# Optimization experiments

Hardware: AMD Instinct MI355X
Metric: run time of the kernel (lower is better)

The kernel has to match this reference:

```python
import jax, jax.numpy as jnp
import numpy as np

B, N, E, H = 2, 2048, 1024, 16
HD = E // H  # head_dim = 64


def setup_inputs() -> dict:
    key = jax.random.key(0)
    k1, k2, k3, k4, k5 = jax.random.split(key, 5)
    x = jax.random.normal(k1, (B, N, E), dtype=jnp.float32)
    # per-head Linear(E, 3*HD): stacked weights [H, E, 3*HD] and biases [H, 3*HD]
    Wqkv = jax.random.normal(k2, (H, E, 3 * HD), dtype=jnp.float32) * (1.0 / np.sqrt(E))
    bqkv = jax.random.normal(k3, (H, 3 * HD), dtype=jnp.float32) * 0.01
    Wout = jax.random.normal(k4, (E, E), dtype=jnp.float32) * (1.0 / np.sqrt(E))
    bout = jax.random.normal(k5, (E,), dtype=jnp.float32) * 0.01
    return {"x": x, "Wqkv": Wqkv, "bqkv": bqkv, "Wout": Wout, "bout": bout}


def reference(x, Wqkv, bqkv, Wout, bout):
    # per-head QKV projection, vectorized over heads: [B, H, N, 3*HD]
    proj = jnp.einsum('bne,hef->bhnf', x, Wqkv) + bqkv[None, :, None, :]
    k, q, v = jnp.split(proj, 3, axis=-1)  # each [B, H, N, HD]
    # scores = q @ k^T / sqrt(HD): [B, H, N, N]
    scores = jnp.einsum('bhqd,bhkd->bhqk', q, k) / jnp.sqrt(jnp.asarray(HD, dtype=x.dtype))
    # causal mask (tril)
    causal = jnp.tril(jnp.ones((N, N), dtype=bool))
    scores = jnp.where(causal[None, None, :, :], scores, -jnp.inf)
    attn = jax.nn.softmax(scores, axis=-1)
    sa = jnp.einsum('bhqk,bhkd->bhqd', attn, v)  # [B, H, N, HD]
    # concat heads in order -> [B, N, E]
    sa = jnp.transpose(sa, (0, 2, 1, 3)).reshape(B, N, E)
    return sa @ Wout + bout
```

## Files before the change

### kernel.cpp

```cpp
#include <hip/hip_runtime.h>
#include <hip/hip_bf16.h>

#define Bz 2
#define Nn 2048
#define Ee 1024
#define Hh 16
#define HD 64

typedef unsigned short u16;
typedef unsigned int u32;

typedef __bf16 bf16x8 __attribute__((ext_vector_type(8)));
typedef float f32x4 __attribute__((ext_vector_type(4)));

#define QK_SCALE 0.18033688f

__device__ __forceinline__ float bf2f(u16 u) {
    u32 v = ((u32)u) << 16;
    return __builtin_bit_cast(float, v);
}
__device__ __forceinline__ u16 f2bf(float f) {
    u32 i = __builtin_bit_cast(u32, f);
    u32 r = (i + 0x7FFFu + ((i >> 16) & 1u)) >> 16;
    return (u16)r;
}
__device__ __forceinline__ u32 pack2(float a, float b) {
    return (u32)f2bf(a) | ((u32)f2bf(b) << 16);
}
__device__ __forceinline__ u32 pack2h(float a, float b) {
    u32 ua = __builtin_bit_cast(u32, a) + 0x8000u;
    u32 ub = __builtin_bit_cast(u32, b) + 0x8000u;
    return (ua >> 16) | (ub & 0xFFFF0000u);
}
__device__ __forceinline__ bf16x8 ld_frag(const u16* p) {
    return __builtin_bit_cast(bf16x8, *(const uint4*)p);
}
__device__ __forceinline__ f32x4 zero4() {
    f32x4 z; z[0]=0.f; z[1]=0.f; z[2]=0.f; z[3]=0.f; return z;
}

__device__ __forceinline__ void async_copy16(const u16* g, u16* l) {
    __builtin_amdgcn_global_load_lds(
        (const __attribute__((address_space(1))) u32*)g,
        (__attribute__((address_space(3))) u32*)l, 16, 0, 0);
}

__global__ void ws_diag(float* out, float code) { out[0] = code; }

__global__ __launch_bounds__(256) void convert_x(
    const float* __restrict__ x, u16* __restrict__ xbf)
{
    size_t idx = ((size_t)blockIdx.x * 256 + threadIdx.x) * 8;
    float4 f0 = *(const float4*)(x + idx);
    float4 f1 = *(const float4*)(x + idx + 4);
    uint4 pk;
    pk.x = pack2(f0.x, f0.y); pk.y = pack2(f0.z, f0.w);
    pk.z = pack2(f1.x, f1.y); pk.w = pack2(f1.z, f1.w);
    *(uint4*)(xbf + idx) = pk;
}

__global__ __launch_bounds__(256) void transpose_f32_bf16(
    const float* __restrict__ src, u16* __restrict__ dst, int R, int C)
{
    const int r0 = blockIdx.x * 64, c0 = blockIdx.y * 64;
    const size_t zoff = (size_t)blockIdx.z * R * C;
    src += zoff; dst += zoff;
    const int tid = threadIdx.x;

    __shared__ float T[64][65];
    {
        int tr = tid >> 2, tc = (tid & 3) * 16;
        const float* s = src + (size_t)(r0 + tr) * C + c0 + tc;
#pragma unroll
        for (int j = 0; j < 4; ++j) {
            float4 v = ((const float4*)s)[j];
            T[tr][tc + 4 * j + 0] = v.x; T[tr][tc + 4 * j + 1] = v.y;
            T[tr][tc + 4 * j + 2] = v.z; T[tr][tc + 4 * j + 3] = v.w;
        }
    }
    __syncthreads();
    {
        int cc = tid >> 2, rr = (tid & 3) * 16;
        u16* d = dst + (size_t)(c0 + cc) * R + r0 + rr;
        u32 w[8];
#pragma unroll
        for (int i = 0; i < 8; ++i)
            w[i] = pack2(T[rr + 2 * i][cc], T[rr + 2 * i + 1][cc]);
        *(uint4*)(d)     = make_uint4(w[0], w[1], w[2], w[3]);
        *(uint4*)(d + 8) = make_uint4(w[4], w[5], w[6], w[7]);
    }
}

__global__ __launch_bounds__(256) void transpose_v(
    const u16* __restrict__ src, u16* __restrict__ dst)
{
    const int n0 = blockIdx.x * 64;
    const size_t z = blockIdx.y;
    src += z * (size_t)Nn * HD;
    dst += z * (size_t)HD * Nn;
    const int tid = threadIdx.x;

    __shared__ u16 T[64][66];
    {
        int tr = tid >> 2, tc = (tid & 3) * 16;
        const u16* s = src + (size_t)(n0 + tr) * HD + tc;
        *(uint4*)&T[tr][tc]     = *(const uint4*)(s);
        *(uint4*)&T[tr][tc + 8] = *(const uint4*)(s + 8);
    }
    __syncthreads();
    {
        int cc = tid >> 2, rr = (tid & 3) * 16;
        u32 w[8];
#pragma unroll
        for (int i = 0; i < 8; ++i)
            w[i] = (u32)T[rr + 2 * i][cc] | ((u32)T[rr + 2 * i + 1][cc] << 16);
        u16* d = dst + (size_t)cc * Nn + n0 + rr;
        *(uint4*)(d)     = make_uint4(w[0], w[1], w[2], w[3]);
        *(uint4*)(d + 8) = make_uint4(w[4], w[5], w[6], w[7]);
    }
}

__global__ __launch_bounds__(256) void qkv_mfma(
    const u16* __restrict__ xbf, const u16* __restrict__ Wt,
    const float* __restrict__ bias,
    u16* __restrict__ kbuf, u16* __restrict__ qbuf, u16* __restrict__ vbuf)
{
    const int mt = blockIdx.x;
    const int h  = blockIdx.y;
    const int tid = threadIdx.x;
    const int lane = tid & 63, wid = tid >> 6;
    const int wy = wid >> 1, wx = wid & 1;
    const int quad = lane >> 4, l15 = lane & 15;

    __shared__ u16 As[128 * 64];
    __shared__ u16 Bs[192 * 64];

    f32x4 acc[4][6];
#pragma unroll
    for (int mi = 0; mi < 4; ++mi)
#pragma unroll
        for (int ni = 0; ni < 6; ++ni) acc[mi][ni] = zero4();

    const u16* xb = xbf + (size_t)mt * 128 * Ee;
    const u16* wtb = Wt + (size_t)h * 192 * 1024;

    const int arowl = lane >> 3;
    const int jj = (lane & 7) ^ arowl;

    for (int kb = 0; kb < 16; ++kb) {
        __syncthreads();
#pragma unroll
        for (int i = 0; i < 4; ++i) {
            int rbase = (wid * 4 + i) * 8;
            const u16* g = xb + (size_t)(rbase + arowl) * Ee + kb * 64 + jj * 8;
            async_copy16(g, &As[(wid * 4 + i) * 512]);
        }
#pragma unroll
        for (int i = 0; i < 6; ++i) {
            int rbase = (wid * 6 + i) * 8;
            const u16* g = wtb + (size_t)(rbase + arowl) * 1024 + kb * 64 + jj * 8;
            async_copy16(g, &Bs[(wid * 6 + i) * 512]);
        }
        __syncthreads();

#pragma unroll
        for (int kk0 = 0; kk0 < 2; ++kk0) {
            const int pos = ((kk0 * 4 + quad) ^ (l15 & 7)) * 8;
            bf16x8 af[4], bf[6];
#pragma unroll
            for (int mi = 0; mi < 4; ++mi)
                af[mi] = ld_frag(&As[(wy * 64 + mi * 16 + l15) * 64 + pos]);
#pragma unroll
            for (int ni = 0; ni < 6; ++ni)
                bf[ni] = ld_frag(&Bs[(wx * 96 + ni * 16 + l15) * 64 + pos]);
#pragma unroll
            for (int mi = 0; mi < 4; ++mi)
#pragma unroll
                for (int ni = 0; ni < 6; ++ni)
                    acc[mi][ni] = __builtin_amdgcn_mfma_f32_16x16x32_bf16(
                        af[mi], bf[ni], acc[mi][ni], 0, 0, 0);
        }
    }

#pragma unroll
    for (int ni = 0; ni < 6; ++ni) {
        int col = wx * 96 + ni * 16 + l15;
        int ft = col >> 6, d = col & 63;
        u16* dst = (ft == 0) ? kbuf : (ft == 1) ? qbuf : vbuf;
        float sc = (ft == 1) ? QK_SCALE : 1.0f;
        float bv = bias[h * 192 + col];
#pragma unroll
        for (int mi = 0; mi < 4; ++mi)
#pragma unroll
            for (int r = 0; r < 4; ++r) {
                int gm = mt * 128 + wy * 64 + mi * 16 + quad * 4 + r;
                int bb = gm >> 11, n = gm & (Nn - 1);
                dst[(((size_t)(bb * Hh + h)) * Nn + n) * HD + d] =
                    f2bf((acc[mi][ni][r] + bv) * sc);
            }
    }
}

__global__ __launch_bounds__(256) void attn2(
    const u16* __restrict__ qbuf, const u16* __restrict__ kbuf,
    const u16* __restrict__ vtb, u16* __restrict__ p0buf,
    u16* __restrict__ p1buf, float* __restrict__ ml)
{
    const int id = blockIdx.x;
    const int bh = (id & 7) * 4 + ((id >> 3) & 3);
    const int p  = id >> 5;
    const int tid = threadIdx.x;
    const int lane = tid & 63, wid = tid >> 6;
    const int l15 = lane & 15, quad = lane >> 4;

    __shared__ u16 KsL[2][4096];
    __shared__ u16 VtL[2][4096];

    const u16* qb = qbuf + (size_t)bh * Nn * HD;
    const u16* kb = kbuf + (size_t)bh * Nn * HD;
    const u16* vt = vtb + (size_t)bh * HD * Nn;

    const int r_l = lane >> 3;
    const int jj = (lane & 7) ^ r_l;
    const int xsw = l15 & 7;
    const int src0 = l15 + (quad & 1) * 32;
    const bool qhi = quad >= 2;

    for (int sg = 0; sg < 2; ++sg) {
        const int qt = sg ? (31 - p) : p;
        const int T  = qt + 1;
        const int t0 = sg ? ((T + 1) >> 1) : 0;
        const int t1 = sg ? T : ((p + 2) >> 1);
        u16*   pb = sg ? p1buf : p0buf;
        float* mb = ml + (sg ? 131072 : 0);
        float* lb = ml + (sg ? 196608 : 65536);

        const int qrow = qt * 64 + wid * 16 + l15;

        f32x4 oacc[4];
#pragma unroll
        for (int dt = 0; dt < 4; ++dt) oacc[dt] = zero4();
        float m_i = -3e38f, l_i = 0.f;

        if (t0 < t1) {
            bf16x8 qf[2];
#pragma unroll
            for (int st = 0; st < 2; ++st)
                qf[st] = __builtin_bit_cast(bf16x8,
                    *(const uint4*)(qb + (size_t)qrow * HD + st * 32 + quad * 8));

            __syncthreads();
#pragma unroll
            for (int i2 = 0; i2 < 4; ++i2) {
                int idx = wid * 4 + i2;
                if (idx < 8) {
                    const u16* g = kb + (size_t)(t0 * 64 + idx * 8 + r_l) * HD + jj * 8;
                    async_copy16(g, &KsL[0][idx * 512]);
                } else {
                    int ii = idx - 8;
                    const u16* g = vt + (size_t)(ii * 8 + r_l) * Nn + t0 * 64 + jj * 8;
                    async_copy16(g, &VtL[0][ii * 512]);
                }
            }

            const int nit = t1 - t0;
            for (int i = 0; i < nit; ++i) {
                const int tk = t0 + i;
                __syncthreads();
                if (i + 1 < nit) {
                    const int nb = (i + 1) & 1;
#pragma unroll
                    for (int i2 = 0; i2 < 4; ++i2) {
                        int idx = wid * 4 + i2;
                        if (idx < 8) {
                            const u16* g = kb + (size_t)((tk + 1) * 64 + idx * 8 + r_l) * HD + jj * 8;
                            async_copy16(g, &KsL[nb][idx * 512]);
                        } else {
                            int ii = idx - 8;
                            const u16* g = vt + (size_t)(ii * 8 + r_l) * Nn + (tk + 1) * 64 + jj * 8;
                            async_copy16(g, &VtL[nb][ii * 512]);
                        }
                    }
                }
                const u16* K = KsL[i & 1];
                const u16* V = VtL[i & 1];

                f32x4 s[4];
#pragma unroll
                for (int t = 0; t < 4; ++t) {
                    f32x4 a = zero4();
#pragma unroll
                    for (int st = 0; st < 2; ++st) {
                        bf16x8 kf = ld_frag(&K[(t * 16 + l15) * 64 +
                                               ((st * 4 + quad) ^ xsw) * 8]);
                        a = __builtin_amdgcn_mfma_f32_16x16x32_bf16(kf, qf[st], a, 0, 0, 0);
                    }
                    s[t] = a;
                }

                if (tk == qt) {
#pragma unroll
                    for (int t = 0; t < 4; ++t)
#pragma unroll
                        for (int r = 0; r < 4; ++r) {
                            int key = tk * 64 + t * 16 + quad * 4 + r;
                            if (key > qrow) s[t][r] = -3e38f;
                        }
                }

                float mx = s[0][0];
#pragma unroll
                for (int t = 0; t < 4; ++t)
#pragma unroll
                    for (int r = 0; r < 4; ++r) mx = fmaxf(mx, s[t][r]);
                mx = fmaxf(mx, __shfl_xor(mx, 16));
                mx = fmaxf(mx, __shfl_xor(mx, 32));
                float mn = fmaxf(m_i, mx);
                float alpha = exp2f(m_i - mn);
                m_i = mn;
                float rs = 0.f;
#pragma unroll
                for (int t = 0; t < 4; ++t)
#pragma unroll
                    for (int r = 0; r < 4; ++r) {
                        float e = exp2f(s[t][r] - mn);
                        s[t][r] = e;
                        rs += e;
                    }
                rs += __shfl_xor(rs, 16);
                rs += __shfl_xor(rs, 32);
                l_i = l_i * alpha + rs;
#pragma unroll
                for (int dt = 0; dt < 4; ++dt)
#pragma unroll
                    for (int r = 0; r < 4; ++r) oacc[dt][r] *= alpha;

                u32 pk[4][2];
#pragma unroll
                for (int t = 0; t < 4; ++t) {
                    pk[t][0] = pack2h(s[t][0], s[t][1]);
                    pk[t][1] = pack2h(s[t][2], s[t][3]);
                }
#pragma unroll
                for (int st = 0; st < 2; ++st) {
                    u32 e0 = pk[2 * st][0],     e1 = pk[2 * st][1];
                    u32 o0 = pk[2 * st + 1][0], o1 = pk[2 * st + 1][1];
                    u32 A0 = __shfl(e0, src0),      B0 = __shfl(o0, src0);
                    u32 A1 = __shfl(e1, src0),      B1 = __shfl(o1, src0);
                    u32 A2 = __shfl(e0, src0 + 16), B2 = __shfl(o0, src0 + 16);
                    u32 A3 = __shfl(e1, src0 + 16), B3 = __shfl(o1, src0 + 16);
                    u32 U0 = qhi ? B0 : A0;
                    u32 U1 = qhi ? B1 : A1;
                    u32 U2 = qhi ? B2 : A2;
                    u32 U3 = qhi ? B3 : A3;
                    bf16x8 pf = __builtin_bit_cast(bf16x8, make_uint4(U0, U1, U2, U3));
#pragma unroll
                    for (int dt = 0; dt < 4; ++dt) {
                        bf16x8 vf = ld_frag(&V[(dt * 16 + l15) * 64 +
                                               ((st * 4 + quad) ^ xsw) * 8]);
                        oacc[dt] = __builtin_amdgcn_mfma_f32_16x16x32_bf16(
                            vf, pf, oacc[dt], 0, 0, 0);
                    }
                }
            }
        }

#pragma unroll
        for (int dt = 0; dt < 4; ++dt) {
            ushort4 ov;
            ov.x = f2bf(oacc[dt][0]);
            ov.y = f2bf(oacc[dt][1]);
            ov.z = f2bf(oacc[dt][2]);
            ov.w = f2bf(oacc[dt][3]);
            *(ushort4*)&pb[((size_t)bh * Nn + qrow) * HD + dt * 16 + quad * 4] = ov;
        }
        if (quad == 0) {
            mb[bh * Nn + qrow] = m_i;
            lb[bh * Nn + qrow] = l_i;
        }
    }
}

__global__ __launch_bounds__(256) void attn_merge(
    const u16* __restrict__ p0, u16* __restrict__ p1,
    const float* __restrict__ ml)
{
    const int idx = blockIdx.x * 256 + threadIdx.x;
    const int row = idx >> 3;
    const int dc = (idx & 7) * 8;

    const float m1 = ml[row],          l1 = ml[65536 + row];
    const float m2 = ml[131072 + row], l2 = ml[196608 + row];
    const float m = fmaxf(m1, m2);
    const float a1 = exp2f(m1 - m), a2 = exp2f(m2 - m);
    const float inv = 1.f / (a1 * l1 + a2 * l2);
    const float s1 = a1 * inv, s2 = a2 * inv;

    const size_t off = (size_t)row * HD + dc;
    uint4 v0 = *(const uint4*)&p0[off];
    uint4 v1 = *(const uint4*)&p1[off];
    u32 a[4] = {v0.x, v0.y, v0.z, v0.w};
    u32 b[4] = {v1.x, v1.y, v1.z, v1.w};
    u32 w[4];
#pragma unroll
    for (int j = 0; j < 4; ++j) {
        float x0 = bf2f((u16)a[j]) * s1 + bf2f((u16)b[j]) * s2;
        float x1 = bf2f((u16)(a[j] >> 16)) * s1 + bf2f((u16)(b[j] >> 16)) * s2;
        w[j] = pack2(x0, x1);
    }
    *(uint4*)&p1[off] = make_uint4(w[0], w[1], w[2], w[3]);
}

typedef float f32x16 __attribute__((ext_vector_type(16)));
__device__ __forceinline__ f32x16 zero16() {
    f32x16 z;
#pragma unroll
    for (int i = 0; i < 16; ++i) z[i] = 0.f;
    return z;
}

__global__ __launch_bounds__(256) void out_mfma(
    const u16* __restrict__ A, const u16* __restrict__ Wt,
    const float* __restrict__ bias, float* __restrict__ out)
{
    const int mt = blockIdx.x;
    const int nt = blockIdx.y;
    const int tid = threadIdx.x;
    const int lane = tid & 63, wid = tid >> 6;
    const int l31 = lane & 31, khalf = (lane >> 5) * 8;

    __shared__ u16 As[128][72];
    __shared__ u16 Bs[64][72];

    f32x16 acc[2];
    acc[0] = zero16(); acc[1] = zero16();

    const int arow = tid >> 1, akh = (tid & 1) * 32;
    const int gm = mt * 128 + arow;
    const int bb = gm >> 11, n = gm & (Nn - 1);
    const int brow = tid >> 2, bc = (tid & 3) * 16;

    for (int k0 = 0; k0 < Ee; k0 += 64) {
        __syncthreads();
        {
            const int c = k0 + akh;
            const int h = c >> 6, d0 = c & 63;
            const u16* asrc = A + (((size_t)(bb * Hh + h) * Nn + n) * HD + d0);
#pragma unroll
            for (int j = 0; j < 4; ++j)
                *(uint4*)&As[arow][akh + 8 * j] = *(const uint4*)(asrc + 8 * j);
            const u16* bsrc = Wt + (size_t)(nt * 64 + brow) * 1024 + k0 + bc;
            *(uint4*)&Bs[brow][bc]     = *(const uint4*)(bsrc);
            *(uint4*)&Bs[brow][bc + 8] = *(const uint4*)(bsrc + 8);
        }
        __syncthreads();
#pragma unroll
        for (int kc = 0; kc < 4; ++kc) {
            bf16x8 af = ld_frag(&As[wid * 32 + l31][kc * 16 + khalf]);
#pragma unroll
            for (int ct = 0; ct < 2; ++ct) {
                bf16x8 bf = ld_frag(&Bs[ct * 32 + l31][kc * 16 + khalf]);
                acc[ct] = __builtin_amdgcn_mfma_f32_32x32x16_bf16(af, bf, acc[ct], 0, 0, 0);
            }
        }
    }

#pragma unroll
    for (int ct = 0; ct < 2; ++ct) {
        int col = nt * 64 + ct * 32 + l31;
        float bv = bias[col];
#pragma unroll
        for (int r = 0; r < 16; ++r) {
            int row_l = (r & 3) + 8 * (r >> 2) + 4 * (lane >> 5);
            int gm2 = mt * 128 + wid * 32 + row_l;
            out[(size_t)gm2 * Ee + col] = acc[ct][r] + bv;
        }
    }
}

extern "C" void kernel_launch(void* const* d_in, const int* in_sizes, int n_in,
                              void* d_out, int out_size, void* d_ws, size_t ws_size,
                              hipStream_t stream) {
    const float* x    = (const float*)d_in[0];
    const float* Wqkv = (const float*)d_in[1];
    const float* bqkv = (const float*)d_in[2];
    const float* Wout = (const float*)d_in[3];
    const float* bout = (const float*)d_in[4];
    float* out = (float*)d_out;

    const size_t SZ = (size_t)Bz * Hh * Nn * HD;
    const size_t NSA = (size_t)Bz * Nn * Ee;
    const size_t NEED = (3 * SZ + NSA) * sizeof(u16);

    if (ws_size < NEED) {
        ws_diag<<<1, 1, 0, stream>>>(out, 20000.0f + (float)(ws_size >> 20));
        return;
    }

    u16* ws = (u16*)d_ws;
    u16* kbuf  = ws;
    u16* qbuf  = ws + SZ;
    u16* vbuf  = ws + 2 * SZ;
    u16* sabuf = ws + 3 * SZ;
    u16* wqkv_t = sabuf;
    u16* wout_t = kbuf;
    u16* xbf    = (u16*)d_out;
    u16* vtb    = (u16*)d_out + SZ;
    u16* p0     = (u16*)d_out;
    u16* p1     = vbuf;
    float* ml   = (float*)sabuf;

    convert_x<<<2048, 256, 0, stream>>>(x, xbf);
    transpose_f32_bf16<<<dim3(16, 3, 16), 256, 0, stream>>>(Wqkv, wqkv_t, 1024, 192);
    qkv_mfma<<<dim3(32, 16), 256, 0, stream>>>(xbf, wqkv_t, bqkv, kbuf, qbuf, vbuf);
    transpose_v<<<dim3(32, 32), 256, 0, stream>>>(vbuf, vtb);
    attn2<<<dim3(1024), 256, 0, stream>>>(qbuf, kbuf, vtb, p0, p1, ml);
    attn_merge<<<dim3(2048), 256, 0, stream>>>(p0, p1, ml);
    transpose_f32_bf16<<<dim3(16, 16, 1), 256, 0, stream>>>(Wout, wout_t, 1024, 1024);
    out_mfma<<<dim3(32, 16), 256, 0, stream>>>(p1, wout_t, bout, out);
}
```

Measured before the change: 196.9 us.

## Fuse prep kernels, write V transposed from QKV GEMM, async-load out GEMM

Merges the x conversion and both weight transposes into one prep launch. The QKV GEMM now writes V directly in transposed layout, which removes the separate transpose_v kernel. The output GEMM switches to global_load_lds async copies into an XOR-swizzled LDS layout. The bf16 pack in attention uses a single perm instruction. This removes three launches and one global round trip for V, but the transposed V stores are 8-byte scattered writes, and Wout's transposed copy gets its own workspace region so its transpose can run earlier.

```diff
diff --git a/kernel.cpp b/kernel.cpp
--- a/kernel.cpp
+++ b/kernel.cpp
@@ -27,10 +27,10 @@
 __device__ __forceinline__ u32 pack2(float a, float b) {
     return (u32)f2bf(a) | ((u32)f2bf(b) << 16);
 }
-__device__ __forceinline__ u32 pack2h(float a, float b) {
+__device__ __forceinline__ u32 pack2p(float a, float b) {
     u32 ua = __builtin_bit_cast(u32, a) + 0x8000u;
     u32 ub = __builtin_bit_cast(u32, b) + 0x8000u;
-    return (ua >> 16) | (ub & 0xFFFF0000u);
+    return __builtin_amdgcn_perm(ub, ua, 0x07060302u);
 }
 __device__ __forceinline__ bf16x8 ld_frag(const u16* p) {
     return __builtin_bit_cast(bf16x8, *(const uint4*)p);
@@ -47,27 +47,39 @@
 
 __global__ void ws_diag(float* out, float code) { out[0] = code; }
 
-__global__ __launch_bounds__(256) void convert_x(
-    const float* __restrict__ x, u16* __restrict__ xbf)
+__global__ __launch_bounds__(256) void prep(
+    const float* __restrict__ x, u16* __restrict__ xbf,
+    const float* __restrict__ Wqkv, u16* __restrict__ wqkv_t,
+    const float* __restrict__ Wout, u16* __restrict__ wout_t)
 {
-    size_t idx = ((size_t)blockIdx.x * 256 + threadIdx.x) * 8;
-    float4 f0 = *(const float4*)(x + idx);
-    float4 f1 = *(const float4*)(x + idx + 4);
-    uint4 pk;
-    pk.x = pack2(f0.x, f0.y); pk.y = pack2(f0.z, f0.w);
-    pk.z = pack2(f1.x, f1.y); pk.w = pack2(f1.z, f1.w);
-    *(uint4*)(xbf + idx) = pk;
-}
-
-__global__ __launch_bounds__(256) void transpose_f32_bf16(
-    const float* __restrict__ src, u16* __restrict__ dst, int R, int C)
-{
-    const int r0 = blockIdx.x * 64, c0 = blockIdx.y * 64;
-    const size_t zoff = (size_t)blockIdx.z * R * C;
-    src += zoff; dst += zoff;
+    const int id = blockIdx.x;
     const int tid = threadIdx.x;
-
     __shared__ float T[64][65];
+
+    if (id < 2048) {
+        size_t idx = ((size_t)id * 256 + tid) * 8;
+        float4 f0 = *(const float4*)(x + idx);
+        float4 f1 = *(const float4*)(x + idx + 4);
+        uint4 pk;
+        pk.x = pack2(f0.x, f0.y); pk.y = pack2(f0.z, f0.w);
+        pk.z = pack2(f1.x, f1.y); pk.w = pack2(f1.z, f1.w);
+        *(uint4*)(xbf + idx) = pk;
+        return;
+    }
+
+    const float* src; u16* dst; int R, C, r0, c0;
+    if (id < 2816) {
+        int j = id - 2048;
+        R = 1024; C = 192;
+        r0 = (j & 15) * 64; c0 = ((j >> 4) % 3) * 64;
+        size_t zoff = (size_t)(j / 48) * R * C;
+        src = Wqkv + zoff; dst = wqkv_t + zoff;
+    } else {
+        int j = id - 2816;
+        R = 1024; C = 1024;
+        r0 = (j & 15) * 64; c0 = (j >> 4) * 64;
+        src = Wout; dst = wout_t;
+    }
     {
         int tr = tid >> 2, tc = (tid & 3) * 16;
         const float* s = src + (size_t)(r0 + tr) * C + c0 + tc;
@@ -91,39 +103,10 @@
     }
 }
 
-__global__ __launch_bounds__(256) void transpose_v(
-    const u16* __restrict__ src, u16* __restrict__ dst)
-{
-    const int n0 = blockIdx.x * 64;
-    const size_t z = blockIdx.y;
-    src += z * (size_t)Nn * HD;
-    dst += z * (size_t)HD * Nn;
-    const int tid = threadIdx.x;
-
-    __shared__ u16 T[64][66];
-    {
-        int tr = tid >> 2, tc = (tid & 3) * 16;
-        const u16* s = src + (size_t)(n0 + tr) * HD + tc;
-        *(uint4*)&T[tr][tc]     = *(const uint4*)(s);
-        *(uint4*)&T[tr][tc + 8] = *(const uint4*)(s + 8);
-    }
-    __syncthreads();
-    {
-        int cc = tid >> 2, rr = (tid & 3) * 16;
-        u32 w[8];
-#pragma unroll
-        for (int i = 0; i < 8; ++i)
-            w[i] = (u32)T[rr + 2 * i][cc] | ((u32)T[rr + 2 * i + 1][cc] << 16);
-        u16* d = dst + (size_t)cc * Nn + n0 + rr;
-        *(uint4*)(d)     = make_uint4(w[0], w[1], w[2], w[3]);
-        *(uint4*)(d + 8) = make_uint4(w[4], w[5], w[6], w[7]);
-    }
-}
-
 __global__ __launch_bounds__(256) void qkv_mfma(
     const u16* __restrict__ xbf, const u16* __restrict__ Wt,
     const float* __restrict__ bias,
-    u16* __restrict__ kbuf, u16* __restrict__ qbuf, u16* __restrict__ vbuf)
+    u16* __restrict__ kbuf, u16* __restrict__ qbuf, u16* __restrict__ vtb)
 {
     const int mt = blockIdx.x;
     const int h  = blockIdx.y;
@@ -186,18 +169,27 @@
     for (int ni = 0; ni < 6; ++ni) {
         int col = wx * 96 + ni * 16 + l15;
         int ft = col >> 6, d = col & 63;
-        u16* dst = (ft == 0) ? kbuf : (ft == 1) ? qbuf : vbuf;
         float sc = (ft == 1) ? QK_SCALE : 1.0f;
         float bv = bias[h * 192 + col];
 #pragma unroll
-        for (int mi = 0; mi < 4; ++mi)
-#pragma unroll
-            for (int r = 0; r < 4; ++r) {
-                int gm = mt * 128 + wy * 64 + mi * 16 + quad * 4 + r;
-                int bb = gm >> 11, n = gm & (Nn - 1);
-                dst[(((size_t)(bb * Hh + h)) * Nn + n) * HD + d] =
-                    f2bf((acc[mi][ni][r] + bv) * sc);
+        for (int mi = 0; mi < 4; ++mi) {
+            int gmb = mt * 128 + wy * 64 + mi * 16 + quad * 4;
+            int bb = gmb >> 11, n = gmb & (Nn - 1);
+            if (ft == 2) {
+                ushort4 ov;
+                ov.x = f2bf(acc[mi][ni][0] + bv);
+                ov.y = f2bf(acc[mi][ni][1] + bv);
+                ov.z = f2bf(acc[mi][ni][2] + bv);
+                ov.w = f2bf(acc[mi][ni][3] + bv);
+                *(ushort4*)&vtb[((size_t)(bb * Hh + h) * HD + d) * Nn + n] = ov;
+            } else {
+                u16* dst = (ft == 0) ? kbuf : qbuf;
+#pragma unroll
+                for (int r = 0; r < 4; ++r)
+                    dst[(((size_t)(bb * Hh + h)) * Nn + (n + r)) * HD + d] =
+                        f2bf((acc[mi][ni][r] + bv) * sc);
             }
+        }
     }
 }
 
@@ -338,8 +330,8 @@
                 u32 pk[4][2];
 #pragma unroll
                 for (int t = 0; t < 4; ++t) {
-                    pk[t][0] = pack2h(s[t][0], s[t][1]);
-                    pk[t][1] = pack2h(s[t][2], s[t][3]);
+                    pk[t][0] = pack2p(s[t][0], s[t][1]);
+                    pk[t][1] = pack2p(s[t][2], s[t][3]);
                 }
 #pragma unroll
                 for (int st = 0; st < 2; ++st) {
@@ -427,39 +419,41 @@
     const int nt = blockIdx.y;
     const int tid = threadIdx.x;
     const int lane = tid & 63, wid = tid >> 6;
-    const int l31 = lane & 31, khalf = (lane >> 5) * 8;
-
-    __shared__ u16 As[128][72];
-    __shared__ u16 Bs[64][72];
+    const int l31 = lane & 31, half = lane >> 5;
+
+    __shared__ u16 As[128 * 64];
+    __shared__ u16 Bs[64 * 64];
 
     f32x16 acc[2];
     acc[0] = zero16(); acc[1] = zero16();
 
-    const int arow = tid >> 1, akh = (tid & 1) * 32;
-    const int gm = mt * 128 + arow;
-    const int bb = gm >> 11, n = gm & (Nn - 1);
-    const int brow = tid >> 2, bc = (tid & 3) * 16;
-
-    for (int k0 = 0; k0 < Ee; k0 += 64) {
+    const int r_l = lane >> 3;
+    const int jj = (lane & 7) ^ r_l;
+
+    for (int kb = 0; kb < 16; ++kb) {
         __syncthreads();
-        {
-            const int c = k0 + akh;
-            const int h = c >> 6, d0 = c & 63;
-            const u16* asrc = A + (((size_t)(bb * Hh + h) * Nn + n) * HD + d0);
-#pragma unroll
-            for (int j = 0; j < 4; ++j)
-                *(uint4*)&As[arow][akh + 8 * j] = *(const uint4*)(asrc + 8 * j);
-            const u16* bsrc = Wt + (size_t)(nt * 64 + brow) * 1024 + k0 + bc;
-            *(uint4*)&Bs[brow][bc]     = *(const uint4*)(bsrc);
-            *(uint4*)&Bs[brow][bc + 8] = *(const uint4*)(bsrc + 8);
+#pragma unroll
+        for (int i = 0; i < 4; ++i) {
+            int row = (wid * 4 + i) * 8 + r_l;
+            int gm = mt * 128 + row;
+            int bb = gm >> 11, n = gm & (Nn - 1);
+            const u16* g = A + ((size_t)(bb * Hh + kb) * Nn + n) * HD + jj * 8;
+            async_copy16(g, &As[(wid * 4 + i) * 512]);
+        }
+#pragma unroll
+        for (int i = 0; i < 2; ++i) {
+            int row = (wid * 2 + i) * 8 + r_l;
+            const u16* g = Wt + (size_t)(nt * 64 + row) * 1024 + kb * 64 + jj * 8;
+            async_copy16(g, &Bs[(wid * 2 + i) * 512]);
         }
         __syncthreads();
 #pragma unroll
         for (int kc = 0; kc < 4; ++kc) {
-            bf16x8 af = ld_frag(&As[wid * 32 + l31][kc * 16 + khalf]);
+            const int pa = ((kc * 2 + half) ^ (l31 & 7)) * 8;
+            bf16x8 af = ld_frag(&As[(wid * 32 + l31) * 64 + pa]);
 #pragma unroll
             for (int ct = 0; ct < 2; ++ct) {
-                bf16x8 bf = ld_frag(&Bs[ct * 32 + l31][kc * 16 + khalf]);
+                bf16x8 bf = ld_frag(&Bs[(ct * 32 + l31) * 64 + pa]);
                 acc[ct] = __builtin_amdgcn_mfma_f32_32x32x16_bf16(af, bf, acc[ct], 0, 0, 0);
             }
         }
@@ -471,7 +465,7 @@
         float bv = bias[col];
 #pragma unroll
         for (int r = 0; r < 16; ++r) {
-            int row_l = (r & 3) + 8 * (r >> 2) + 4 * (lane >> 5);
+            int row_l = (r & 3) + 8 * (r >> 2) + 4 * half;
             int gm2 = mt * 128 + wid * 32 + row_l;
             out[(size_t)gm2 * Ee + col] = acc[ct][r] + bv;
         }
@@ -503,19 +497,16 @@
     u16* vbuf  = ws + 2 * SZ;
     u16* sabuf = ws + 3 * SZ;
     u16* wqkv_t = sabuf;
-    u16* wout_t = kbuf;
+    u16* wout_t = sabuf + 16 * 192 * 1024;
     u16* xbf    = (u16*)d_out;
     u16* vtb    = (u16*)d_out + SZ;
     u16* p0     = (u16*)d_out;
     u16* p1     = vbuf;
     float* ml   = (float*)sabuf;
 
-    convert_x<<<2048, 256, 0, stream>>>(x, xbf);
-    transpose_f32_bf16<<<dim3(16, 3, 16), 256, 0, stream>>>(Wqkv, wqkv_t, 1024, 192);
-    qkv_mfma<<<dim3(32, 16), 256, 0, stream>>>(xbf, wqkv_t, bqkv, kbuf, qbuf, vbuf);
-    transpose_v<<<dim3(32, 32), 256, 0, stream>>>(vbuf, vtb);
+    prep<<<dim3(3072), 256, 0, stream>>>(x, xbf, Wqkv, wqkv_t, Wout, wout_t);
+    qkv_mfma<<<dim3(32, 16), 256, 0, stream>>>(xbf, wqkv_t, bqkv, kbuf, qbuf, vtb);
     attn2<<<dim3(1024), 256, 0, stream>>>(qbuf, kbuf, vtb, p0, p1, ml);
     attn_merge<<<dim3(2048), 256, 0, stream>>>(p0, p1, ml);
-    transpose_f32_bf16<<<dim3(16, 16, 1), 256, 0, stream>>>(Wout, wout_t, 1024, 1024);
     out_mfma<<<dim3(32, 16), 256, 0, stream>>>(p1, wout_t, bout, out);
 }
```

New measurement: 209.2 us. +6.3%, slower.
